# Optimization experiments

Hardware: AMD Instinct MI355X
Metric: run time of the kernel (lower is better)

The kernel has to match this reference:

```python
import jax, jax.numpy as jnp
import numpy as np

TOP_N = 10
N_HEADS = 8

def _layernorm(x, g, b, eps=1e-5):
    mu = jnp.mean(x, axis=-1, keepdims=True)
    var = jnp.mean((x - mu) ** 2, axis=-1, keepdims=True)
    return (x - mu) * jax.lax.rsqrt(var + eps) * g + b

def setup_inputs() -> dict:
    key = jax.random.key(0)
    ks = jax.random.split(key, 16)
    B, N, D = 4096, 32768, 512
    s = 1.0 / np.sqrt(D)
    inp = {
        "visit_rep": jax.random.normal(ks[0], (B, D), jnp.float32),
        "E_mem_patient_rep": jax.random.normal(ks[1], (N, D), jnp.float32),
        "E_mem_med_rep": jax.random.normal(ks[2], (N, D), jnp.float32),
        "Wq": jax.random.uniform(ks[3], (D, D), jnp.float32, -s, s),
        "Wk": jax.random.uniform(ks[4], (D, D), jnp.float32, -s, s),
        "Wv": jax.random.uniform(ks[5], (D, D), jnp.float32, -s, s),
        "bq": jnp.zeros((D,), jnp.float32),
        "bk": jnp.zeros((D,), jnp.float32),
        "bv": jnp.zeros((D,), jnp.float32),
        "Wo": jax.random.uniform(ks[6], (D, D), jnp.float32, -s, s),
        "bo": jnp.zeros((D,), jnp.float32),
        "W1": jax.random.uniform(ks[7], (D, D), jnp.float32, -s, s),
        "b1": jax.random.uniform(ks[8], (D,), jnp.float32, -s, s),
        "W2": jax.random.uniform(ks[9], (D, D), jnp.float32, -s, s),
        "b2": jax.random.uniform(ks[10], (D,), jnp.float32, -s, s),
        "ln1_g": jnp.ones((D,), jnp.float32),
        "ln1_b": jnp.zeros((D,), jnp.float32),
        "ln2_g": jnp.ones((D,), jnp.float32),
        "ln2_b": jnp.zeros((D,), jnp.float32),
    }
    return inp

def reference(visit_rep, E_mem_patient_rep, E_mem_med_rep,
              Wq, bq, Wk, bk, Wv, bv, Wo, bo,
              W1, b1, W2, b2, ln1_g, ln1_b, ln2_g, ln2_b):
    B, D = visit_rep.shape
    H = N_HEADS
    hd = D // H
    # --- exact L2 kNN (faiss GpuIndexFlatL2 equivalent), detached ---
    q = jax.lax.stop_gradient(visit_rep)
    M = jax.lax.stop_gradient(E_mem_patient_rep)
    d2 = (jnp.sum(q * q, axis=1, keepdims=True)
          - 2.0 * q @ M.T
          + jnp.sum(M * M, axis=1)[None, :])          # [B, N]
    _, I = jax.lax.top_k(-d2, TOP_N)                    # [B, top_n]
    k = E_mem_patient_rep[I]                            # [B, top_n, D]
    v = E_mem_med_rep[I]                                # [B, top_n, D]
    # --- multihead attention, query seq-len 1 ---
    qh = (visit_rep @ Wq.T + bq).reshape(B, H, hd)
    kh = (k @ Wk.T + bk).reshape(B, TOP_N, H, hd)
    vh = (v @ Wv.T + bv).reshape(B, TOP_N, H, hd)
    scores = jnp.einsum("bhd,bnhd->bhn", qh, kh) / np.sqrt(hd)
    attn = jax.nn.softmax(scores, axis=-1)
    ctx = jnp.einsum("bhn,bnhd->bhd", attn, vh).reshape(B, D)
    attn_out = ctx @ Wo.T + bo
    # --- residual + norms + FFN (dropout = identity in eval) ---
    x = _layernorm(visit_rep + attn_out, ln1_g, ln1_b)
    ff = (jax.nn.leaky_relu(x @ W1.T + b1, 0.01)) @ W2.T + b2
    x = _layernorm(x + ff, ln2_g, ln2_b)
    return x
```

## Files before the change

kernel.cpp:

```cpp
#include <hip/hip_runtime.h>
#include <math.h>

#define BQ 4096
#define NMEM 32768
#define DD 512
#define TOPN 10
#define NBX 128
#define ENT 2048
#define NCF 16
#define LK 6
#define FINF 3.402823466e+38f
#define IMAX 0x7fffffff

typedef __attribute__((ext_vector_type(8))) short    bf16x8;
typedef __attribute__((ext_vector_type(4))) float    f32x4;

__device__ __forceinline__ unsigned short f2bf(float x) {
    unsigned int u = __float_as_uint(x);
    u += 0x7fffu + ((u >> 16) & 1u);
    return (unsigned short)(u >> 16);
}
__device__ __forceinline__ void async_copy16(const void* gp, void* lp) {
    __builtin_amdgcn_global_load_lds(
        (const __attribute__((address_space(1))) void*)gp,
        (__attribute__((address_space(3))) void*)lp, 16, 0, 0);
}
__device__ __forceinline__ bool lt_si(float s, int j, float s2, int j2) {
    return (s < s2) || (s == s2 && j < j2);
}
template<int KN>
__device__ __forceinline__ void topk_insert(float (&ts)[KN], int (&ti)[KN], float s, int j) {
    if (!lt_si(s, j, ts[KN-1], ti[KN-1])) return;
    #pragma unroll
    for (int p = KN-1; p > 0; --p) {
        if (lt_si(s, j, ts[p-1], ti[p-1])) { ts[p] = ts[p-1]; ti[p] = ti[p-1]; }
        else { ts[p] = s; ti[p] = j; return; }
    }
    ts[0] = s; ti[0] = j;
}

struct CastDesc {
    const float* in[7];
    unsigned short* out[7];
    int start[8];
};
__global__ __launch_bounds__(256) void cast_multi_kernel(CastDesc d) {
    int blk = blockIdx.x;
    int seg = 0;
    #pragma unroll
    for (int s = 0; s < 6; ++s) seg += (blk >= d.start[s + 1]) ? 1 : 0;
    int local = blk - d.start[seg];
    int i = (local * 256 + threadIdx.x) * 4;
    float4 v = *(const float4*)(d.in[seg] + i);
    ushort4 o;
    o.x = f2bf(v.x); o.y = f2bf(v.y); o.z = f2bf(v.z); o.w = f2bf(v.w);
    *(ushort4*)(d.out[seg] + i) = o;
}

__global__ __launch_bounds__(256) void cast_norm2_kernel(
        const float* __restrict__ inA, unsigned short* __restrict__ outA,
        const float* __restrict__ inB, unsigned short* __restrict__ outB,
        float* __restrict__ mnorm) {
    const float* in = blockIdx.y ? inB : inA;
    unsigned short* out = blockIdx.y ? outB : outA;
    int row = blockIdx.x * 4 + (threadIdx.x >> 6);
    int lane = threadIdx.x & 63;
    const float* r = in + (size_t)row * DD + lane * 8;
    float4 a = *(const float4*)r;
    float4 b = *(const float4*)(r + 4);
    ushort4 oa, ob;
    oa.x = f2bf(a.x); oa.y = f2bf(a.y); oa.z = f2bf(a.z); oa.w = f2bf(a.w);
    ob.x = f2bf(b.x); ob.y = f2bf(b.y); ob.z = f2bf(b.z); ob.w = f2bf(b.w);
    unsigned short* op = out + (size_t)row * DD + lane * 8;
    *(ushort4*)op = oa; *(ushort4*)(op + 4) = ob;
    if (blockIdx.y == 0) {
        float s = a.x*a.x + a.y*a.y + a.z*a.z + a.w*a.w
                + b.x*b.x + b.y*b.y + b.z*b.z + b.w*b.w;
        #pragma unroll
        for (int off = 32; off; off >>= 1) s += __shfl_xor(s, off, 64);
        if (lane == 0) mnorm[row] = s;
    }
}

__global__ __launch_bounds__(512, 2) void gemm_knn_kernel(
        const unsigned short* __restrict__ Qb,
        const unsigned short* __restrict__ Mb,
        const float* __restrict__ mnorm,
        unsigned* __restrict__ cand_part) {
    __shared__ __align__(16) union {
        struct { unsigned short A[4][256][32]; unsigned short B[4][256][32]; } g;
        unsigned S[64 * 260];
    } sh;
    const int tid  = threadIdx.x;
    const int lane = tid & 63;
    const int wave = tid >> 6;
    const int quad = lane >> 4, c16 = lane & 15;
    const int wm = wave >> 2, wn = wave & 3;
    const int m0 = blockIdx.y * 256, n0 = blockIdx.x * 256;
    const int srow   = tid >> 2;
    const int schunk = (tid & 3) ^ ((tid >> 3) & 3);
    const unsigned short* ag = Qb + (size_t)(m0 + srow) * DD + schunk * 8;
    const unsigned short* bg = Mb + (size_t)(n0 + srow) * DD + schunk * 8;
    const int cq = (quad ^ ((c16 >> 1) & 3)) * 8;

    f32x4  acc[8][4] = {};
    bf16x8 af[4], bf[4];

#define STG_A(tt) do {                                                          \
    const int s_ = (tt) & 3;                                                    \
    async_copy16(ag + (tt)*32,           &sh.g.A[s_][srow][(tid & 3) * 8]);     \
    async_copy16(ag + (tt)*32 + 128*DD,  &sh.g.A[s_][128 + srow][(tid & 3) * 8]);\
} while (0)
#define STG_B(tt) do {                                                          \
    const int s_ = (tt) & 3;                                                    \
    async_copy16(bg + (tt)*32,           &sh.g.B[s_][srow][(tid & 3) * 8]);     \
    async_copy16(bg + (tt)*32 + 128*DD,  &sh.g.B[s_][128 + srow][(tid & 3) * 8]);\
} while (0)
#define RD_A(tt, mh) do {                                                       \
    const int s_ = (tt) & 3;                                                    \
    _Pragma("unroll")                                                           \
    for (int mt2 = 0; mt2 < 4; ++mt2)                                           \
        af[mt2] = *(const bf16x8*)&sh.g.A[s_][wm*128 + ((mh)*4 + mt2)*16 + c16][cq];\
} while (0)
#define RD_B(tt) do {                                                           \
    const int s_ = (tt) & 3;                                                    \
    _Pragma("unroll")                                                           \
    for (int nt = 0; nt < 4; ++nt)                                              \
        bf[nt] = *(const bf16x8*)&sh.g.B[s_][wn*64 + nt*16 + c16][cq];          \
} while (0)
#define MM(mh) do {                                                             \
    _Pragma("unroll")                                                           \
    for (int mt2 = 0; mt2 < 4; ++mt2)                                           \
        _Pragma("unroll")                                                       \
        for (int nt = 0; nt < 4; ++nt)                                          \
            acc[(mh)*4 + mt2][nt] = __builtin_amdgcn_mfma_f32_16x16x32_bf16(    \
                af[mt2], bf[nt], acc[(mh)*4 + mt2][nt], 0, 0, 0);               \
} while (0)

    STG_A(0); STG_B(0); STG_A(1); STG_B(1); STG_A(2); STG_B(2);
    asm volatile("s_waitcnt vmcnt(8)" ::: "memory");
    __builtin_amdgcn_s_barrier();
    __builtin_amdgcn_sched_barrier(0);

    #pragma unroll
    for (int t = 0; t < 16; ++t) {
        RD_A(t, 0); RD_B(t);
        if (t + 3 < 16) STG_A(t + 3);
        __builtin_amdgcn_sched_barrier(0);
        __builtin_amdgcn_s_barrier();
        asm volatile("s_waitcnt lgkmcnt(0)" ::: "memory");
        __builtin_amdgcn_sched_barrier(0);
        __builtin_amdgcn_s_setprio(1);
        MM(0);
        __builtin_amdgcn_s_setprio(0);
        __builtin_amdgcn_sched_barrier(0);
        __builtin_amdgcn_s_barrier();
        RD_A(t, 1);
        if (t + 3 < 16) STG_B(t + 3);
        if (t <= 12)      asm volatile("s_waitcnt vmcnt(8)" ::: "memory");
        else if (t == 13) asm volatile("s_waitcnt vmcnt(4)" ::: "memory");
        else if (t == 14) asm volatile("s_waitcnt vmcnt(0)" ::: "memory");
        __builtin_amdgcn_sched_barrier(0);
        __builtin_amdgcn_s_barrier();
        asm volatile("s_waitcnt lgkmcnt(0)" ::: "memory");
        __builtin_amdgcn_sched_barrier(0);
        __builtin_amdgcn_s_setprio(1);
        MM(1);
        __builtin_amdgcn_s_setprio(0);
        __builtin_amdgcn_sched_barrier(0);
        __builtin_amdgcn_s_barrier();
    }
#undef STG_A
#undef STG_B
#undef RD_A
#undef RD_B
#undef MM

    float mn[4];
    #pragma unroll
    for (int nt = 0; nt < 4; ++nt) mn[nt] = mnorm[n0 + wn*64 + nt*16 + c16];
    const int rrow = tid >> 1, rhalf = tid & 1;
    __syncthreads();
    #pragma unroll
    for (int p = 0; p < 4; ++p) {
        if (wn == p) {
            #pragma unroll
            for (int mt = 0; mt < 8; ++mt)
                #pragma unroll
                for (int nt = 0; nt < 4; ++nt) {
                    uint4 w;
                    #pragma unroll
                    for (int r = 0; r < 4; ++r) {
                        float s = fmaxf(fmaf(-2.f, acc[mt][nt][r], mn[nt]), 0.f);
                        (&w.x)[r] = (__float_as_uint(s) & 0xFFFFFF80u)
                                  | (unsigned)((p & 1) * 64 + nt * 16 + c16);
                    }
                    *(uint4*)&sh.S[(nt*16 + c16) * 260 + wm*128 + mt*16 + quad*4] = w;
                }
        }
        __syncthreads();
        unsigned q4[4] = {0xFFFFFFFFu, 0xFFFFFFFFu, 0xFFFFFFFFu, 0xFFFFFFFFu};
        #pragma unroll
        for (int m = 0; m < 32; ++m) {
            unsigned nv = sh.S[(rhalf*32 + m) * 260 + rrow];
            #pragma unroll
            for (int i = 0; i < 4; ++i) {
                unsigned lo = min(q4[i], nv);
                nv = max(q4[i], nv);
                q4[i] = lo;
            }
        }
        unsigned p0 = (unsigned)__shfl_xor((int)q4[0], 1, 64);
        unsigned p1 = (unsigned)__shfl_xor((int)q4[1], 1, 64);
        unsigned p2 = (unsigned)__shfl_xor((int)q4[2], 1, 64);
        unsigned p3 = (unsigned)__shfl_xor((int)q4[3], 1, 64);
        if (rhalf == 0) {
            uint4 w4;
            w4.x = min(q4[0], p3); w4.y = min(q4[1], p2);
            w4.z = min(q4[2], p1); w4.w = min(q4[3], p0);
            *(uint4*)(cand_part + (size_t)(m0 + rrow) * ENT + blockIdx.x * 16 + p * 4) = w4;
        }
        __syncthreads();
    }
}

__global__ __launch_bounds__(256) void knn_select_kernel(
        const unsigned* __restrict__ cand_part,
        const float* __restrict__ Q, const float* __restrict__ Mm,
        const float* __restrict__ mnorm,
        int* __restrict__ knn_idx) {
    const int row = blockIdx.x;
    const int wave = threadIdx.x >> 6, lane = threadIdx.x & 63;
    __shared__ unsigned sk[64];
    __shared__ int      sc[64];
    __shared__ int      ids[NCF];
    __shared__ float    d2s[NCF];

    unsigned ks[LK]; int ti[LK];
    #pragma unroll
    for (int q = 0; q < LK; ++q) { ks[q] = 0xFFFFFFFFu; ti[q] = IMAX; }
    const uint4* p4 = (const uint4*)(cand_part + (size_t)row * ENT) + wave * 128;
    #pragma unroll
    for (int i = 0; i < 2; ++i) {
        uint4 v = p4[lane + 64 * i];
        #pragma unroll
        for (int e = 0; e < 4; ++e) {
            unsigned k = (&v.x)[e];
            int pos = wave * 512 + (lane + 64 * i) * 4 + e;
            int gcol = (pos >> 3) * 128 + (int)(k & 127u);
            bool cm[LK];
            #pragma unroll
            for (int q = 0; q < LK; ++q) cm[q] = k < ks[q];
            #pragma unroll
            for (int q = LK - 1; q > 0; --q) {
                unsigned tns = cm[q] ? k : ks[q];  int tni = cm[q] ? gcol : ti[q];
                ks[q] = cm[q-1] ? ks[q-1] : tns;
                ti[q] = cm[q-1] ? ti[q-1] : tni;
            }
            ks[0] = cm[0] ? k : ks[0];
            ti[0] = cm[0] ? gcol : ti[0];
        }
    }
    #pragma unroll
    for (int r = 0; r < NCF; ++r) {
        unsigned mk = ks[0]; int mi = ti[0];
        #pragma unroll
        for (int off = 1; off < 64; off <<= 1) {
            unsigned ok = (unsigned)__shfl_xor((int)mk, off, 64);
            int      oi = __shfl_xor(mi, off, 64);
            bool t = (ok < mk) || (ok == mk && oi < mi);
            mk = t ? ok : mk; mi = t ? oi : mi;
        }
        bool win = (ks[0] == mk) && (ti[0] == mi);
        #pragma unroll
        for (int q = 0; q < LK - 1; ++q) {
            ks[q] = win ? ks[q+1] : ks[q];
            ti[q] = win ? ti[q+1] : ti[q];
        }
        ks[LK-1] = win ? 0xFFFFFFFFu : ks[LK-1];
        ti[LK-1] = win ? IMAX : ti[LK-1];
        if (lane == r) { sk[wave * NCF + r] = mk; sc[wave * NCF + r] = mi; }
    }
    __syncthreads();
    if (wave == 0) {
        unsigned myk = sk[lane];
        int      myc = sc[lane];
        #pragma unroll
        for (int r = 0; r < NCF; ++r) {
            unsigned mk = myk; int mi = myc;
            #pragma unroll
            for (int off = 1; off < 64; off <<= 1) {
                unsigned ok = (unsigned)__shfl_xor((int)mk, off, 64);
                int      oi = __shfl_xor(mi, off, 64);
                bool t = (ok < mk) || (ok == mk && oi < mi);
                mk = t ? ok : mk; mi = t ? oi : mi;
            }
            bool win = (myk == mk) && (myc == mi);
            myk = win ? 0xFFFFFFFFu : myk;
            myc = win ? IMAX : myc;
            if (lane == r) ids[r] = mi;
        }
    }
    __syncthreads();
    float4 q0 = *(const float4*)(Q + (size_t)row * DD + lane * 8);
    float4 q1 = *(const float4*)(Q + (size_t)row * DD + lane * 8 + 4);
    for (int c = wave; c < NCF; c += 4) {
        int j = ids[c];
        const float* mr = Mm + (size_t)j * DD;
        float4 m0 = *(const float4*)(mr + lane * 8);
        float4 m1 = *(const float4*)(mr + lane * 8 + 4);
        float dot = q0.x*m0.x + q0.y*m0.y + q0.z*m0.z + q0.w*m0.w
                  + q1.x*m1.x + q1.y*m1.y + q1.z*m1.z + q1.w*m1.w;
        #pragma unroll
        for (int off = 32; off; off >>= 1) dot += __shfl_xor(dot, off, 64);
        if (lane == 0) d2s[c] = fmaf(-2.f, dot, mnorm[j]);
    }
    __syncthreads();
    if (threadIdx.x == 0) {
        float ts[TOPN]; int tj[TOPN];
        #pragma unroll
        for (int p = 0; p < TOPN; ++p) { ts[p] = FINF; tj[p] = IMAX; }
        for (int c = 0; c < NCF; ++c) topk_insert<TOPN>(ts, tj, d2s[c], ids[c]);
        #pragma unroll
        for (int p = 0; p < TOPN; ++p) knn_idx[row * TOPN + p] = tj[p];
    }
}

template<int ACT, int OUT_BF16>
__global__ __launch_bounds__(256) void gemm_bf16_nt(
        const unsigned short* __restrict__ A,
        const unsigned short* __restrict__ B,
        const float* __restrict__ bias,
        void* __restrict__ Cout, int ldc) {
    __shared__ __align__(16) unsigned short As[128 * 64];
    __shared__ __align__(16) unsigned short Bs[128 * 64];
    const int tid  = threadIdx.x;
    const int wave = tid >> 6, lane = tid & 63;
    const int quad = lane >> 4, c16 = lane & 15;
    const int m0 = blockIdx.y * 128, n0 = blockIdx.x * 128;
    const int wm0 = (wave >> 1) * 64, wn0 = (wave & 1) * 64;
    const int srow = wave * 32 + (lane >> 3);
    const int schunk = (lane & 7) ^ ((lane >> 3) & 7);
    const int xsw = c16 & 7;

    f32x4 acc[4][4] = {};

    for (int kt = 0; kt < DD; kt += 64) {
        __syncthreads();
        #pragma unroll
        for (int i = 0; i < 4; ++i) {
            const unsigned short* ga = A + (size_t)(m0 + srow + i * 8) * DD + kt + schunk * 8;
            async_copy16(ga, &As[(wave * 32 + i * 8) * 64]);
            const unsigned short* gb = B + (size_t)(n0 + srow + i * 8) * DD + kt + schunk * 8;
            async_copy16(gb, &Bs[(wave * 32 + i * 8) * 64]);
        }
        __syncthreads();
        #pragma unroll
        for (int ks = 0; ks < 64; ks += 32) {
            const int coff = (((ks >> 3) + quad) ^ xsw) << 3;
            bf16x8 af[4], bff[4];
            #pragma unroll
            for (int mt = 0; mt < 4; ++mt)
                af[mt] = *(const bf16x8*)&As[(wm0 + mt * 16 + c16) * 64 + coff];
            #pragma unroll
            for (int nt = 0; nt < 4; ++nt)
                bff[nt] = *(const bf16x8*)&Bs[(wn0 + nt * 16 + c16) * 64 + coff];
            #pragma unroll
            for (int mt = 0; mt < 4; ++mt)
                #pragma unroll
                for (int nt = 0; nt < 4; ++nt)
                    acc[mt][nt] = __builtin_amdgcn_mfma_f32_16x16x32_bf16(
                        af[mt], bff[nt], acc[mt][nt], 0, 0, 0);
        }
    }
    #pragma unroll
    for (int nt = 0; nt < 4; ++nt) {
        int ncol = n0 + wn0 + nt * 16 + c16;
        float bv = bias[ncol];
        #pragma unroll
        for (int mt = 0; mt < 4; ++mt) {
            size_t rbase = (size_t)(m0 + wm0 + mt * 16 + quad * 4) * ldc + ncol;
            #pragma unroll
            for (int r = 0; r < 4; ++r) {
                float v = acc[mt][nt][r] + bv;
                if (ACT == 1) v = v >= 0.f ? v : 0.01f * v;
                if (OUT_BF16) ((unsigned short*)Cout)[rbase + (size_t)r * ldc] = f2bf(v);
                else          ((float*)Cout)[rbase + (size_t)r * ldc] = v;
            }
        }
    }
}

struct G3 {
    const unsigned short* A[3];
    const unsigned short* B[3];
    const float* bias[3];
    void* C[3];
    int obf[3];
};
__global__ __launch_bounds__(256) void gemm3_kernel(G3 g) {
    const int yy = blockIdx.y;
    const int z = (yy >= 512) ? 2 : (yy >= 256 ? 1 : 0);
    const int my = yy - z * 256;
    __shared__ __align__(16) unsigned short As[128 * 64];
    __shared__ __align__(16) unsigned short Bs[128 * 64];
    const unsigned short* A = g.A[z];
    const unsigned short* B = g.B[z];
    const int tid  = threadIdx.x;
    const int wave = tid >> 6, lane = tid & 63;
    const int quad = lane >> 4, c16 = lane & 15;
    const int m0 = my * 128, n0 = blockIdx.x * 128;
    const int wm0 = (wave >> 1) * 64, wn0 = (wave & 1) * 64;
    const int srow = wave * 32 + (lane >> 3);
    const int schunk = (lane & 7) ^ ((lane >> 3) & 7);
    const int xsw = c16 & 7;

    f32x4 acc[4][4] = {};

    for (int kt = 0; kt < DD; kt += 64) {
        __syncthreads();
        #pragma unroll
        for (int i = 0; i < 4; ++i) {
            const unsigned short* ga = A + (size_t)(m0 + srow + i * 8) * DD + kt + schunk * 8;
            async_copy16(ga, &As[(wave * 32 + i * 8) * 64]);
            const unsigned short* gb = B + (size_t)(n0 + srow + i * 8) * DD + kt + schunk * 8;
            async_copy16(gb, &Bs[(wave * 32 + i * 8) * 64]);
        }
        __syncthreads();
        #pragma unroll
        for (int ks = 0; ks < 64; ks += 32) {
            const int coff = (((ks >> 3) + quad) ^ xsw) << 3;
            bf16x8 af[4], bff[4];
            #pragma unroll
            for (int mt = 0; mt < 4; ++mt)
                af[mt] = *(const bf16x8*)&As[(wm0 + mt * 16 + c16) * 64 + coff];
            #pragma unroll
            for (int nt = 0; nt < 4; ++nt)
                bff[nt] = *(const bf16x8*)&Bs[(wn0 + nt * 16 + c16) * 64 + coff];
            #pragma unroll
            for (int mt = 0; mt < 4; ++mt)
                #pragma unroll
                for (int nt = 0; nt < 4; ++nt)
                    acc[mt][nt] = __builtin_amdgcn_mfma_f32_16x16x32_bf16(
                        af[mt], bff[nt], acc[mt][nt], 0, 0, 0);
        }
    }
    const int obf = g.obf[z];
    #pragma unroll
    for (int nt = 0; nt < 4; ++nt) {
        int ncol = n0 + wn0 + nt * 16 + c16;
        float bv = g.bias[z][ncol];
        #pragma unroll
        for (int mt = 0; mt < 4; ++mt) {
            size_t rbase = (size_t)(m0 + wm0 + mt * 16 + quad * 4) * DD + ncol;
            #pragma unroll
            for (int r = 0; r < 4; ++r) {
                float v = acc[mt][nt][r] + bv;
                if (obf) ((unsigned short*)g.C[z])[rbase + (size_t)r * DD] = f2bf(v);
                else     ((float*)g.C[z])[rbase + (size_t)r * DD] = v;
            }
        }
    }
}

__global__ __launch_bounds__(512) void attn_kernel(
        const float* __restrict__ qh, const unsigned short* __restrict__ Kall,
        const unsigned short* __restrict__ Vall, const int* __restrict__ knn_idx,
        unsigned short* __restrict__ ctx_b) {
    const int b = blockIdx.x;
    const int h = threadIdx.x >> 6;
    const int l = threadIdx.x & 63;
    const int col = (h << 6) + l;
    int idxs[TOPN];
    #pragma unroll
    for (int n = 0; n < TOPN; ++n) idxs[n] = knn_idx[b * TOPN + n];
    const float q = qh[(size_t)b * DD + col];
    float sc[TOPN];
    #pragma unroll
    for (int n = 0; n < TOPN; ++n) {
        float p = q * __uint_as_float((unsigned)Kall[(size_t)idxs[n] * DD + col] << 16);
        #pragma unroll
        for (int off = 32; off; off >>= 1) p += __shfl_xor(p, off, 64);
        sc[n] = p * 0.125f;
    }
    float mx = sc[0];
    #pragma unroll
    for (int n = 1; n < TOPN; ++n) mx = fmaxf(mx, sc[n]);
    float se = 0.f;
    #pragma unroll
    for (int n = 0; n < TOPN; ++n) { sc[n] = expf(sc[n] - mx); se += sc[n]; }
    const float inv = 1.f / se;
    float o = 0.f;
    #pragma unroll
    for (int n = 0; n < TOPN; ++n)
        o = fmaf(sc[n] * inv,
                 __uint_as_float((unsigned)Vall[(size_t)idxs[n] * DD + col] << 16), o);
    ctx_b[(size_t)b * DD + col] = f2bf(o);
}

template<int EMIT_BF16>
__global__ __launch_bounds__(256) void add_ln_kernel(
        const float* __restrict__ X, const float* __restrict__ Y,
        const float* __restrict__ g, const float* __restrict__ be,
        float* __restrict__ out, unsigned short* __restrict__ out_b) {
    const int row = blockIdx.x;
    const int t = threadIdx.x;
    const size_t base = (size_t)row * DD;
    float v0 = X[base + t]       + Y[base + t];
    float v1 = X[base + 256 + t] + Y[base + 256 + t];
    float s = v0 + v1, sq = v0 * v0 + v1 * v1;
    #pragma unroll
    for (int off = 32; off; off >>= 1) { s += __shfl_xor(s, off, 64); sq += __shfl_xor(sq, off, 64); }
    __shared__ float rs[4], rq[4];
    const int w = t >> 6, l = t & 63;
    if (l == 0) { rs[w] = s; rq[w] = sq; }
    __syncthreads();
    float tot  = rs[0] + rs[1] + rs[2] + rs[3];
    float totq = rq[0] + rq[1] + rq[2] + rq[3];
    float mu = tot * (1.f / DD);
    float var = totq * (1.f / DD) - mu * mu;
    float rstd = rsqrtf(var + 1e-5f);
    float o0 = (v0 - mu) * rstd * g[t]       + be[t];
    float o1 = (v1 - mu) * rstd * g[256 + t] + be[256 + t];
    out[base + t] = o0;
    out[base + 256 + t] = o1;
    if (EMIT_BF16) {
        out_b[base + t] = f2bf(o0);
        out_b[base + 256 + t] = f2bf(o1);
    }
}

extern "C" void kernel_launch(void* const* d_in, const int* in_sizes, int n_in,
                              void* d_out, int out_size, void* d_ws, size_t ws_size,
                              hipStream_t stream) {
    const float* visit = (const float*)d_in[0];
    const float* Epat  = (const float*)d_in[1];
    const float* Emed  = (const float*)d_in[2];
    const float* Wq = (const float*)d_in[3];
    const float* Wk = (const float*)d_in[4];
    const float* Wv = (const float*)d_in[5];
    const float* bq = (const float*)d_in[6];
    const float* bk = (const float*)d_in[7];
    const float* bv = (const float*)d_in[8];
    const float* Wo = (const float*)d_in[9];
    const float* bo = (const float*)d_in[10];
    const float* W1 = (const float*)d_in[11];
    const float* b1 = (const float*)d_in[12];
    const float* W2 = (const float*)d_in[13];
    const float* b2 = (const float*)d_in[14];
    const float* ln1g = (const float*)d_in[15];
    const float* ln1b = (const float*)d_in[16];
    const float* ln2g = (const float*)d_in[17];
    const float* ln2b = (const float*)d_in[18];
    float* out = (float*)d_out;

    char* base = (char*)d_ws;
    const size_t MB = 1u << 20;
    float* mnorm   = (float*)(base);
    int*   knn_idx = (int*)  (base + 2*MB);
    float* qh      = (float*)(base + 3*MB);
    float* attn_o  = qh;
    float* x1      = (float*)(base + 11*MB);
    float* ff      = (float*)(base + 19*MB);
    unsigned short* Qb    = (unsigned short*)(base + 27*MB);
    unsigned short* ctx_b = (unsigned short*)(base + 31*MB);
    unsigned short* x1_b  = (unsigned short*)(base + 35*MB);
    unsigned short* h1_b  = (unsigned short*)(base + 39*MB);
    unsigned short* Wq_b  = (unsigned short*)(base + 43*MB);
    unsigned short* Wk_b  = Wq_b + 262144;
    unsigned short* Wv_b  = Wk_b + 262144;
    unsigned short* Wo_b  = Wv_b + 262144;
    unsigned short* W1_b  = Wo_b + 262144;
    unsigned short* W2_b  = W1_b + 262144;
    unsigned short* Mb     = (unsigned short*)(base + 46*MB);
    unsigned short* Emed_b = (unsigned short*)(base + 78*MB);
    unsigned short* Kall = (unsigned short*)(base + 110*MB);
    unsigned short* Vall = Kall + (size_t)NMEM * DD;
    unsigned* cand_part = (unsigned*)Kall;

    cast_norm2_kernel<<<dim3(NMEM / 4, 2), 256, 0, stream>>>(Epat, Mb, Emed, Emed_b, mnorm);
    CastDesc cd;
    cd.in[0] = visit; cd.out[0] = Qb;
    cd.in[1] = Wq; cd.in[2] = Wk; cd.in[3] = Wv; cd.in[4] = Wo; cd.in[5] = W1; cd.in[6] = W2;
    cd.out[1] = Wq_b; cd.out[2] = Wk_b; cd.out[3] = Wv_b; cd.out[4] = Wo_b; cd.out[5] = W1_b; cd.out[6] = W2_b;
    cd.start[0] = 0; cd.start[1] = 2048;
    for (int s = 2; s <= 7; ++s) cd.start[s] = cd.start[s-1] + 256;
    cast_multi_kernel<<<cd.start[7], 256, 0, stream>>>(cd);

    gemm_knn_kernel<<<dim3(NBX, BQ / 256), 512, 0, stream>>>(Qb, Mb, mnorm, cand_part);
    knn_select_kernel<<<BQ, 256, 0, stream>>>(cand_part, visit, Epat, mnorm, knn_idx);

    G3 g3;
    g3.A[0] = Mb;     g3.B[0] = Wk_b; g3.bias[0] = bk; g3.C[0] = Kall; g3.obf[0] = 1;
    g3.A[1] = Emed_b; g3.B[1] = Wv_b; g3.bias[1] = bv; g3.C[1] = Vall; g3.obf[1] = 1;
    g3.A[2] = Qb;     g3.B[2] = Wq_b; g3.bias[2] = bq; g3.C[2] = qh;   g3.obf[2] = 0;
    gemm3_kernel<<<dim3(4, 544), 256, 0, stream>>>(g3);

    attn_kernel<<<BQ, 512, 0, stream>>>(qh, Kall, Vall, knn_idx, ctx_b);

    gemm_bf16_nt<0,0><<<dim3(4, BQ / 128), 256, 0, stream>>>(ctx_b, Wo_b, bo, attn_o, DD);
    add_ln_kernel<1><<<BQ, 256, 0, stream>>>(visit, attn_o, ln1g, ln1b, x1, x1_b);
    gemm_bf16_nt<1,1><<<dim3(4, BQ / 128), 256, 0, stream>>>(x1_b, W1_b, b1, h1_b, DD);
    gemm_bf16_nt<0,0><<<dim3(4, BQ / 128), 256, 0, stream>>>(h1_b, W2_b, b2, ff,   DD);
    add_ln_kernel<0><<<BQ, 256, 0, stream>>>(x1, ff, ln2g, ln2b, out, nullptr);
}
```

Before: 599.0 us.

## Quantize kNN distance GEMM to int8 MFMA with per-row scales

Adds per-row symmetric int8 quantization of the patient memory and the queries inside the cast kernel, and switches the kNN distance GEMM from bf16 MFMA to int8 16x16x64 MFMA with int32 accumulation. Distances are rebuilt from the product of the row scales. The aim is to halve the GEMM operand bytes and K-loop iterations and to use the higher int8 matrix throughput. The candidate prefilter becomes coarser, which relies on the later exact fp32 reselection in knn_select to keep the true top-k. It also adds an extra quantize pass over the queries.

```diff
diff --git a/kernel.cpp b/kernel.cpp
--- a/kernel.cpp
+++ b/kernel.cpp
@@ -14,6 +14,7 @@
 
 typedef __attribute__((ext_vector_type(8))) short    bf16x8;
 typedef __attribute__((ext_vector_type(4))) float    f32x4;
+typedef __attribute__((ext_vector_type(4))) int      i32x4;
 
 __device__ __forceinline__ unsigned short f2bf(float x) {
     unsigned int u = __float_as_uint(x);
@@ -60,37 +61,65 @@
 __global__ __launch_bounds__(256) void cast_norm2_kernel(
         const float* __restrict__ inA, unsigned short* __restrict__ outA,
         const float* __restrict__ inB, unsigned short* __restrict__ outB,
-        float* __restrict__ mnorm) {
-    const float* in = blockIdx.y ? inB : inA;
-    unsigned short* out = blockIdx.y ? outB : outA;
+        const float* __restrict__ inV,
+        signed char* __restrict__ outA8, signed char* __restrict__ outV8,
+        float* __restrict__ mnorm, float* __restrict__ msc,
+        float* __restrict__ qsc) {
+    const int pl = blockIdx.y;
+    if (pl == 2 && blockIdx.x >= BQ / 4) return;
+    const float* in = (pl == 0) ? inA : (pl == 1 ? inB : inV);
     int row = blockIdx.x * 4 + (threadIdx.x >> 6);
     int lane = threadIdx.x & 63;
     const float* r = in + (size_t)row * DD + lane * 8;
     float4 a = *(const float4*)r;
     float4 b = *(const float4*)(r + 4);
-    ushort4 oa, ob;
-    oa.x = f2bf(a.x); oa.y = f2bf(a.y); oa.z = f2bf(a.z); oa.w = f2bf(a.w);
-    ob.x = f2bf(b.x); ob.y = f2bf(b.y); ob.z = f2bf(b.z); ob.w = f2bf(b.w);
-    unsigned short* op = out + (size_t)row * DD + lane * 8;
-    *(ushort4*)op = oa; *(ushort4*)(op + 4) = ob;
-    if (blockIdx.y == 0) {
+    if (pl < 2) {
+        unsigned short* out = pl ? outB : outA;
+        ushort4 oa, ob;
+        oa.x = f2bf(a.x); oa.y = f2bf(a.y); oa.z = f2bf(a.z); oa.w = f2bf(a.w);
+        ob.x = f2bf(b.x); ob.y = f2bf(b.y); ob.z = f2bf(b.z); ob.w = f2bf(b.w);
+        unsigned short* op = out + (size_t)row * DD + lane * 8;
+        *(ushort4*)op = oa; *(ushort4*)(op + 4) = ob;
+    }
+    if (pl != 1) {
+        float ax = fmaxf(fmaxf(fmaxf(fabsf(a.x), fabsf(a.y)), fmaxf(fabsf(a.z), fabsf(a.w))),
+                         fmaxf(fmaxf(fabsf(b.x), fabsf(b.y)), fmaxf(fabsf(b.z), fabsf(b.w))));
         float s = a.x*a.x + a.y*a.y + a.z*a.z + a.w*a.w
                 + b.x*b.x + b.y*b.y + b.z*b.z + b.w*b.w;
         #pragma unroll
-        for (int off = 32; off; off >>= 1) s += __shfl_xor(s, off, 64);
-        if (lane == 0) mnorm[row] = s;
+        for (int off = 32; off; off >>= 1) {
+            ax = fmaxf(ax, __shfl_xor(ax, off, 64));
+            if (pl == 0) s += __shfl_xor(s, off, 64);
+        }
+        ax = fmaxf(ax, 1e-30f);
+        float inv = 127.0f / ax;
+        int q[8];
+        q[0] = __float2int_rn(a.x*inv); q[1] = __float2int_rn(a.y*inv);
+        q[2] = __float2int_rn(a.z*inv); q[3] = __float2int_rn(a.w*inv);
+        q[4] = __float2int_rn(b.x*inv); q[5] = __float2int_rn(b.y*inv);
+        q[6] = __float2int_rn(b.z*inv); q[7] = __float2int_rn(b.w*inv);
+        unsigned w0 = (q[0]&255) | ((q[1]&255)<<8) | ((q[2]&255)<<16) | ((unsigned)(q[3]&255)<<24);
+        unsigned w1 = (q[4]&255) | ((q[5]&255)<<8) | ((q[6]&255)<<16) | ((unsigned)(q[7]&255)<<24);
+        signed char* o8 = (pl == 0 ? outA8 : outV8) + (size_t)row * DD + lane * 8;
+        *(uint2*)o8 = make_uint2(w0, w1);
+        if (lane == 0) {
+            if (pl == 0) { mnorm[row] = s; msc[row] = ax * (1.0f/127.0f); }
+            else         { qsc[row] = ax * (1.0f/127.0f); }
+        }
     }
 }
 
 __global__ __launch_bounds__(512, 2) void gemm_knn_kernel(
-        const unsigned short* __restrict__ Qb,
-        const unsigned short* __restrict__ Mb,
-        const float* __restrict__ mnorm,
+        const signed char* __restrict__ Q8,
+        const signed char* __restrict__ M8,
+        const float* __restrict__ mnorm, const float* __restrict__ msc,
+        const float* __restrict__ qsc,
         unsigned* __restrict__ cand_part) {
     __shared__ __align__(16) union {
-        struct { unsigned short A[4][256][32]; unsigned short B[4][256][32]; } g;
+        struct { signed char A[4][256][64]; signed char B[4][256][64]; } g;
         unsigned S[64 * 260];
     } sh;
+    __shared__ float qs[256];
     const int tid  = threadIdx.x;
     const int lane = tid & 63;
     const int wave = tid >> 6;
@@ -99,41 +128,43 @@
     const int m0 = blockIdx.y * 256, n0 = blockIdx.x * 256;
     const int srow   = tid >> 2;
     const int schunk = (tid & 3) ^ ((tid >> 3) & 3);
-    const unsigned short* ag = Qb + (size_t)(m0 + srow) * DD + schunk * 8;
-    const unsigned short* bg = Mb + (size_t)(n0 + srow) * DD + schunk * 8;
-    const int cq = (quad ^ ((c16 >> 1) & 3)) * 8;
-
-    f32x4  acc[8][4] = {};
-    bf16x8 af[4], bf[4];
+    const signed char* ag = Q8 + (size_t)(m0 + srow) * DD + schunk * 16;
+    const signed char* bg = M8 + (size_t)(n0 + srow) * DD + schunk * 16;
+    const int cq = (quad ^ ((c16 >> 1) & 3)) * 16;
+
+    i32x4 acc[8][4] = {};
+    i32x4 af[4], bf[4];
+
+    if (tid < 256) qs[tid] = qsc[m0 + tid];
 
 #define STG_A(tt) do {                                                          \
     const int s_ = (tt) & 3;                                                    \
-    async_copy16(ag + (tt)*32,           &sh.g.A[s_][srow][(tid & 3) * 8]);     \
-    async_copy16(ag + (tt)*32 + 128*DD,  &sh.g.A[s_][128 + srow][(tid & 3) * 8]);\
+    async_copy16(ag + (size_t)(tt)*64,            &sh.g.A[s_][srow][(tid & 3) * 16]);      \
+    async_copy16(ag + (size_t)(tt)*64 + 128*DD,   &sh.g.A[s_][128 + srow][(tid & 3) * 16]);\
 } while (0)
 #define STG_B(tt) do {                                                          \
     const int s_ = (tt) & 3;                                                    \
-    async_copy16(bg + (tt)*32,           &sh.g.B[s_][srow][(tid & 3) * 8]);     \
-    async_copy16(bg + (tt)*32 + 128*DD,  &sh.g.B[s_][128 + srow][(tid & 3) * 8]);\
+    async_copy16(bg + (size_t)(tt)*64,            &sh.g.B[s_][srow][(tid & 3) * 16]);      \
+    async_copy16(bg + (size_t)(tt)*64 + 128*DD,   &sh.g.B[s_][128 + srow][(tid & 3) * 16]);\
 } while (0)
 #define RD_A(tt, mh) do {                                                       \
     const int s_ = (tt) & 3;                                                    \
     _Pragma("unroll")                                                           \
     for (int mt2 = 0; mt2 < 4; ++mt2)                                           \
-        af[mt2] = *(const bf16x8*)&sh.g.A[s_][wm*128 + ((mh)*4 + mt2)*16 + c16][cq];\
+        af[mt2] = *(const i32x4*)&sh.g.A[s_][wm*128 + ((mh)*4 + mt2)*16 + c16][cq];\
 } while (0)
 #define RD_B(tt) do {                                                           \
     const int s_ = (tt) & 3;                                                    \
     _Pragma("unroll")                                                           \
     for (int nt = 0; nt < 4; ++nt)                                              \
-        bf[nt] = *(const bf16x8*)&sh.g.B[s_][wn*64 + nt*16 + c16][cq];          \
+        bf[nt] = *(const i32x4*)&sh.g.B[s_][wn*64 + nt*16 + c16][cq];           \
 } while (0)
 #define MM(mh) do {                                                             \
     _Pragma("unroll")                                                           \
     for (int mt2 = 0; mt2 < 4; ++mt2)                                           \
         _Pragma("unroll")                                                       \
         for (int nt = 0; nt < 4; ++nt)                                          \
-            acc[(mh)*4 + mt2][nt] = __builtin_amdgcn_mfma_f32_16x16x32_bf16(    \
+            acc[(mh)*4 + mt2][nt] = __builtin_amdgcn_mfma_i32_16x16x64_i8(      \
                 af[mt2], bf[nt], acc[(mh)*4 + mt2][nt], 0, 0, 0);               \
 } while (0)
 
@@ -143,9 +174,9 @@
     __builtin_amdgcn_sched_barrier(0);
 
     #pragma unroll
-    for (int t = 0; t < 16; ++t) {
+    for (int t = 0; t < 8; ++t) {
         RD_A(t, 0); RD_B(t);
-        if (t + 3 < 16) STG_A(t + 3);
+        if (t + 3 < 8) STG_A(t + 3);
         __builtin_amdgcn_sched_barrier(0);
         __builtin_amdgcn_s_barrier();
         asm volatile("s_waitcnt lgkmcnt(0)" ::: "memory");
@@ -156,10 +187,10 @@
         __builtin_amdgcn_sched_barrier(0);
         __builtin_amdgcn_s_barrier();
         RD_A(t, 1);
-        if (t + 3 < 16) STG_B(t + 3);
-        if (t <= 12)      asm volatile("s_waitcnt vmcnt(8)" ::: "memory");
-        else if (t == 13) asm volatile("s_waitcnt vmcnt(4)" ::: "memory");
-        else if (t == 14) asm volatile("s_waitcnt vmcnt(0)" ::: "memory");
+        if (t + 3 < 8) STG_B(t + 3);
+        if (t <= 4)       asm volatile("s_waitcnt vmcnt(8)" ::: "memory");
+        else if (t == 5)  asm volatile("s_waitcnt vmcnt(4)" ::: "memory");
+        else if (t == 6)  asm volatile("s_waitcnt vmcnt(0)" ::: "memory");
         __builtin_amdgcn_sched_barrier(0);
         __builtin_amdgcn_s_barrier();
         asm volatile("s_waitcnt lgkmcnt(0)" ::: "memory");
@@ -176,9 +207,13 @@
 #undef RD_B
 #undef MM
 
-    float mn[4];
-    #pragma unroll
-    for (int nt = 0; nt < 4; ++nt) mn[nt] = mnorm[n0 + wn*64 + nt*16 + c16];
+    float mn[4], ms2[4];
+    #pragma unroll
+    for (int nt = 0; nt < 4; ++nt) {
+        int col = n0 + wn*64 + nt*16 + c16;
+        mn[nt]  = mnorm[col];
+        ms2[nt] = -2.0f * msc[col];
+    }
     const int rrow = tid >> 1, rhalf = tid & 1;
     __syncthreads();
     #pragma unroll
@@ -191,7 +226,9 @@
                     uint4 w;
                     #pragma unroll
                     for (int r = 0; r < 4; ++r) {
-                        float s = fmaxf(fmaf(-2.f, acc[mt][nt][r], mn[nt]), 0.f);
+                        int arow = wm*128 + mt*16 + quad*4 + r;
+                        float coef = ms2[nt] * qs[arow];
+                        float s = fmaxf(fmaf(coef, (float)acc[mt][nt][r], mn[nt]), 0.f);
                         (&w.x)[r] = (__float_as_uint(s) & 0xFFFFFF80u)
                                   | (unsigned)((p & 1) * 64 + nt * 16 + c16);
                     }
@@ -557,6 +594,8 @@
     char* base = (char*)d_ws;
     const size_t MB = 1u << 20;
     float* mnorm   = (float*)(base);
+    float* msc     = (float*)(base + 256*1024);
+    float* qsc     = (float*)(base + 512*1024);
     int*   knn_idx = (int*)  (base + 2*MB);
     float* qh      = (float*)(base + 3*MB);
     float* attn_o  = qh;
@@ -577,8 +616,11 @@
     unsigned short* Kall = (unsigned short*)(base + 110*MB);
     unsigned short* Vall = Kall + (size_t)NMEM * DD;
     unsigned* cand_part = (unsigned*)Kall;
-
-    cast_norm2_kernel<<<dim3(NMEM / 4, 2), 256, 0, stream>>>(Epat, Mb, Emed, Emed_b, mnorm);
+    signed char* M8 = (signed char*)(base + 142*MB);
+    signed char* Q8 = (signed char*)(base + 158*MB);
+
+    cast_norm2_kernel<<<dim3(NMEM / 4, 3), 256, 0, stream>>>(
+        Epat, Mb, Emed, Emed_b, visit, M8, Q8, mnorm, msc, qsc);
     CastDesc cd;
     cd.in[0] = visit; cd.out[0] = Qb;
     cd.in[1] = Wq; cd.in[2] = Wk; cd.in[3] = Wv; cd.in[4] = Wo; cd.in[5] = W1; cd.in[6] = W2;
@@ -587,7 +629,7 @@
     for (int s = 2; s <= 7; ++s) cd.start[s] = cd.start[s-1] + 256;
     cast_multi_kernel<<<cd.start[7], 256, 0, stream>>>(cd);
 
-    gemm_knn_kernel<<<dim3(NBX, BQ / 256), 512, 0, stream>>>(Qb, Mb, mnorm, cand_part);
+    gemm_knn_kernel<<<dim3(NBX, BQ / 256), 512, 0, stream>>>(Q8, M8, mnorm, msc, qsc, cand_part);
     knn_select_kernel<<<BQ, 256, 0, stream>>>(cand_part, visit, Epat, mnorm, knn_idx);
 
     G3 g3;
```

Result: faster. 572.1 us (-4.5%).
